# Optimization experiments

Hardware: AMD Instinct MI355X
Metric: run time of the kernel (lower is better)

The kernel has to match this reference:

```python
import math
import jax, jax.numpy as jnp
import numpy as np

WS = (8, 7, 7)   # window_size (d, h, w)
SS = (4, 3, 3)   # shift_size
NH = 4           # num_heads
DIM = 128


def _rel_position_index(ws):
    # [N*N] int index into the (2wd-1)(2wh-1)(2ww-1) bias table
    cd, ch, cw = np.arange(ws[0]), np.arange(ws[1]), np.arange(ws[2])
    coords = np.stack(np.meshgrid(cd, ch, cw, indexing='ij')).reshape(3, -1)  # [3, N]
    rel = (coords[:, :, None] - coords[:, None, :]).transpose(1, 2, 0)        # [N, N, 3]
    rel[..., 0] += ws[0] - 1
    rel[..., 1] += ws[1] - 1
    rel[..., 2] += ws[2] - 1
    rel[..., 0] *= (2 * ws[1] - 1) * (2 * ws[2] - 1)
    rel[..., 1] *= (2 * ws[2] - 1)
    return rel.sum(-1).reshape(-1)


def _rel_coords_table(ws):
    # [(2wd-1)(2wh-1)(2ww-1), 3] log-spaced continuous coords (Swin v2)
    rd = np.arange(-(ws[0] - 1), ws[0], dtype=np.float32)
    rh = np.arange(-(ws[1] - 1), ws[1], dtype=np.float32)
    rw = np.arange(-(ws[2] - 1), ws[2], dtype=np.float32)
    t = np.stack(np.meshgrid(rd, rh, rw, indexing='ij')).transpose(1, 2, 3, 0)  # [Td,Th,Tw,3]
    t[..., 0] /= ws[0] - 1
    t[..., 1] /= ws[1] - 1
    t[..., 2] /= ws[2] - 1
    t *= 8.0
    t = np.sign(t) * np.log2(np.abs(t) + 1.0) / 3.0
    return t.reshape(-1, 3)


_REL_INDEX = _rel_position_index(WS)
_COORDS = jnp.asarray(_rel_coords_table(WS))


def _attn_mask(pD, pH, pW, ws, ss):
    img = np.zeros((pD, pH, pW), np.float32)
    sl = lambda w, s: (slice(0, -w), slice(-w, -s), slice(-s, None))
    cnt = 0
    for d in sl(ws[0], ss[0]):
        for h in sl(ws[1], ss[1]):
            for w in sl(ws[2], ss[2]):
                img[d, h, w] = cnt
                cnt += 1
    m = img.reshape(pD // ws[0], ws[0], pH // ws[1], ws[1], pW // ws[2], ws[2])
    m = m.transpose(0, 2, 4, 1, 3, 5).reshape(-1, ws[0] * ws[1] * ws[2])  # [nWin, N]
    diff = m[:, None, :] - m[:, :, None]
    return jnp.asarray(np.where(diff != 0, -100.0, 0.0).astype(np.float32))


def setup_inputs() -> dict:
    key = jax.random.key(0)
    ks = jax.random.split(key, 6)
    B, D, H, W, C = 1, 16, 56, 56, DIM
    g = lambda k, shp, sc: jax.random.normal(k, shp, dtype=jnp.float32) * sc
    return {
        'x': g(ks[0], (B, D, H, W, C), 1.0),
        'qkv_weight': g(ks[1], (3 * C, C), 0.02),
        'qkv_bias': jnp.zeros((3 * C,), jnp.float32),
        'proj_weight': g(ks[2], (C, C), 0.02),
        'proj_bias': jnp.zeros((C,), jnp.float32),
        'logit_scale': jnp.full((NH, 1, 1), float(np.log(10.0)), jnp.float32),
        'cpb_w1': g(ks[3], (512, 3), 0.02),
        'cpb_b1': jnp.zeros((512,), jnp.float32),
        'cpb_w2': g(ks[4], (NH, 512), 0.02),
    }


def reference(x, qkv_weight, qkv_bias, proj_weight, proj_bias,
              logit_scale, cpb_w1, cpb_b1, cpb_w2):
    B, D, H, W, C = x.shape
    wd, wh, ww = WS
    hd = C // NH
    pad_d, pad_h, pad_w = (-D) % wd, (-H) % wh, (-W) % ww
    x = jnp.pad(x, ((0, 0), (0, pad_d), (0, pad_h), (0, pad_w), (0, 0)))
    pD, pH, pW = D + pad_d, H + pad_h, W + pad_w
    ss = [0 if WS[i] >= (pD, pH, pW)[i] else SS[i] for i in range(3)]
    shifted = sum(ss) > 0
    if shifted:
        x = jnp.roll(x, (-ss[0], -ss[1], -ss[2]), axis=(1, 2, 3))
    nd, nh, nw = pD // wd, pH // wh, pW // ww
    nWin, N = nd * nh * nw, wd * wh * ww
    # window partition -> [B*nWin, N, C]
    xw = x.reshape(B, nd, wd, nh, wh, nw, ww, C).transpose(0, 1, 3, 5, 2, 4, 6, 7)
    xw = xw.reshape(B * nWin, N, C)
    # qkv with k-bias zeroed (Swin v2 cosine attention)
    qb = qkv_bias.at[C:2 * C].set(0.0)
    qkv = (xw @ qkv_weight.T + qb).reshape(B * nWin, N, 3, NH, hd).transpose(2, 0, 3, 1, 4)
    q, k, v = qkv[0], qkv[1], qkv[2]   # each [B*nWin, NH, N, hd]
    qn = q / jnp.maximum(jnp.linalg.norm(q, axis=-1, keepdims=True), 1e-12)
    kn = k / jnp.maximum(jnp.linalg.norm(k, axis=-1, keepdims=True), 1e-12)
    attn = jnp.einsum('bhnd,bhmd->bhnm', qn, kn)
    scale = jnp.exp(jnp.minimum(logit_scale, math.log(100.0)))  # [NH,1,1]
    attn = attn * scale
    # continuous relative position bias
    table = jax.nn.relu(_COORDS @ cpb_w1.T + cpb_b1) @ cpb_w2.T  # [T, NH]
    bias = table[_REL_INDEX].reshape(N, N, NH).transpose(2, 0, 1)
    bias = 16.0 * jax.nn.sigmoid(bias)
    attn = attn + bias[None]
    if shifted:
        mask = _attn_mask(pD, pH, pW, WS, ss)  # [nWin, N, N]
        attn = attn.reshape(B, nWin, NH, N, N) + mask[None, :, None]
        attn = attn.reshape(B * nWin, NH, N, N)
    attn = jax.nn.softmax(attn, axis=-1)
    out = jnp.einsum('bhnm,bhmd->bhnd', attn, v).transpose(0, 2, 1, 3).reshape(B * nWin, N, C)
    out = out @ proj_weight.T + proj_bias
    # window reverse -> [B, pD, pH, pW, C]
    out = out.reshape(B, nd, nh, nw, wd, wh, ww, C).transpose(0, 1, 4, 2, 5, 3, 6, 7)
    out = out.reshape(B, pD, pH, pW, C)
    if shifted:
        out = jnp.roll(out, tuple(ss), axis=(1, 2, 3))
    return out[:, :D, :H, :W, :]
```

## Files before the change

kernel.cpp:

```cpp
#include <hip/hip_runtime.h>
#include <hip/hip_bf16.h>

typedef unsigned short u16;
typedef unsigned int   u32;
typedef float f32x4  __attribute__((ext_vector_type(4)));
typedef short bf16x8 __attribute__((ext_vector_type(8)));

#define DI __device__ __forceinline__

constexpr int TBL  = 2535;
constexpr int NTOK = 50176;
constexpr float L2E = 1.4426950408889634f;

constexpr int WB_QW = 0;
constexpr int WB_PW = 49152;
constexpr int WB_QB = 65536;
constexpr int WB_PB = 65920;
constexpr int WB_TOT = 66048;

DI float b2f(u16 u){ return __uint_as_float(((u32)u)<<16); }
DI u16 f2b(float f){
  u32 u = __float_as_uint(f);
  return (u16)((u + 0x7fffu + ((u>>16)&1u)) >> 16);
}
DI float ldf(const void* p, int i, int isf32){
  return isf32 ? ((const float*)p)[i] : b2f(((const u16*)p)[i]);
}
DI f32x4 mfma32(bf16x8 a, bf16x8 b, f32x4 c){
  return __builtin_amdgcn_mfma_f32_16x16x32_bf16(a, b, c, 0, 0, 0);
}
DI u32 cvtpk(float lo, float hi){
  u32 r;
  asm("v_cvt_pk_bf16_f32 %0, %1, %2" : "=v"(r) : "v"(lo), "v"(hi));
  return r;
}
DI float vexp2(float x){
  float r;
  asm("v_exp_f32 %0, %1" : "=v"(r) : "v"(x));
  return r;
}
DI int detect_f32(const void* x, int lane){
  u32 w = ((const u32*)x)[lane];
  u16 lo = (u16)w;
  u32 e = (lo >> 7) & 0xFF;
  int wild = (lo != 0 && (e >= 143 || e <= 111)) ? 1 : 0;
  unsigned long long m = __ballot(wild);
  return __popcll(m) > 16;
}

__global__ void k_cpb(const void* __restrict__ w1, const void* __restrict__ b1,
                      const void* __restrict__ w2, const void* __restrict__ x,
                      const void* __restrict__ qw, const void* __restrict__ pw,
                      const void* __restrict__ qb, const void* __restrict__ pb,
                      u16* __restrict__ wb, float* __restrict__ table16){
  const int lane = threadIdx.x;
  const int isf32 = detect_f32(x, lane);
  {
    int gid = blockIdx.x*64 + lane;
    if (gid < WB_TOT){
      const void* src; int off;
      if (gid < WB_PW)      { src = qw; off = gid; }
      else if (gid < WB_QB) { src = pw; off = gid - WB_PW; }
      else if (gid < WB_PB) { src = qb; off = gid - WB_QB; }
      else                  { src = pb; off = gid - WB_PB; }
      wb[gid] = isf32 ? f2b(((const float*)src)[off]) : ((const u16*)src)[off];
    }
  }
  int t = blockIdx.x;
  int i = t/169; int r = t - i*169; int j = r/13; int k = r - j*13;
  float v0 = 8.f*(float)(i-7)/7.f, v1 = 8.f*(float)(j-6)/6.f, v2 = 8.f*(float)(k-6)/6.f;
  float c0 = copysignf(log2f(fabsf(v0)+1.f)*(1.f/3.f), v0);
  float c1 = copysignf(log2f(fabsf(v1)+1.f)*(1.f/3.f), v1);
  float c2 = copysignf(log2f(fabsf(v2)+1.f)*(1.f/3.f), v2);
  float a0=0.f,a1=0.f,a2=0.f,a3=0.f;
  for (int hh = lane; hh < 512; hh += 64){
    float a = c0*ldf(w1,hh*3,isf32) + c1*ldf(w1,hh*3+1,isf32)
            + c2*ldf(w1,hh*3+2,isf32) + ldf(b1,hh,isf32);
    a = fmaxf(a, 0.f);
    a0 += a*ldf(w2,hh,isf32);       a1 += a*ldf(w2,512+hh,isf32);
    a2 += a*ldf(w2,1024+hh,isf32);  a3 += a*ldf(w2,1536+hh,isf32);
  }
  #pragma unroll
  for (int off=32; off; off>>=1){
    a0 += __shfl_xor(a0, off); a1 += __shfl_xor(a1, off);
    a2 += __shfl_xor(a2, off); a3 += __shfl_xor(a3, off);
  }
  if (lane==0){
    table16[t]       = (16.f/(1.f+__expf(-a0)) - 15.f)*L2E;
    table16[TBL+t]   = (16.f/(1.f+__expf(-a1)) - 15.f)*L2E;
    table16[2*TBL+t] = (16.f/(1.f+__expf(-a2)) - 15.f)*L2E;
    table16[3*TBL+t] = (16.f/(1.f+__expf(-a3)) - 15.f)*L2E;
  }
}

__global__ void k_bias(const float* __restrict__ table16, float* __restrict__ bias16){
  int n = blockIdx.x, h = blockIdx.y;
  int td = n/49; int r2 = n - td*49; int th = r2/7; int tw = r2 - th*7;
  const float* tb = table16 + h*TBL;
  float* o = bias16 + ((size_t)h*392 + n)*392;
  for (int m = threadIdx.x; m < 392; m += 128){
    int sd = m/49; int q2 = m - sd*49; int sh = q2/7; int sw = q2 - sh*7;
    int idx = (td - sd + 7)*169 + (th - sh + 6)*13 + (tw - sw + 6);
    o[m] = tb[idx];
  }
}

__global__ __launch_bounds__(256,4) void k_qkv(const void* __restrict__ x,
    const u16* __restrict__ wb, const void* __restrict__ lsc,
    u16* __restrict__ qkvbuf){
  __shared__ __align__(16) u16 Ws[128*136];
  const int tid = threadIdx.x;
  const int lane = tid & 63;
  const int isf32 = detect_f32(x, lane);
  const int wave = tid>>6;
  const int c = lane & 15, g = lane >> 4;
  const int tokbase = blockIdx.x*64 + wave*16;
  bf16x8 ka[4];
  {
    int gtok = tokbase + c;
    int win = gtok/392, tt = gtok - win*392;
    int dwi = win>>6, hwi = (win>>3)&7, wwi = win&7;
    int td = tt/49; int r2 = tt - td*49; int th = r2/7; int tw = r2 - th*7;
    int pd = dwi*8 + td + 4; if (pd >= 16) pd -= 16;
    int ph = hwi*7 + th + 3; if (ph >= 56) ph -= 56;
    int pw = wwi*7 + tw + 3; if (pw >= 56) pw -= 56;
    size_t rowb = (size_t)((pd*56 + ph)*56 + pw)*128;
    if (isf32){
      const float* xr = (const float*)x + rowb + g*8;
      #pragma unroll
      for (int kk=0; kk<4; ++kk){
        float4 f0 = *(const float4*)(xr + kk*32);
        float4 f1 = *(const float4*)(xr + kk*32 + 4);
        uint4 p;
        p.x = cvtpk(f0.x, f0.y);  p.y = cvtpk(f0.z, f0.w);
        p.z = cvtpk(f1.x, f1.y);  p.w = cvtpk(f1.z, f1.w);
        ka[kk] = *(bf16x8*)&p;
      }
    } else {
      const u16* xr = (const u16*)x + rowb + g*8;
      #pragma unroll
      for (int kk=0; kk<4; ++kk)
        ka[kk] = *(const bf16x8*)(xr + kk*32);
    }
  }
  float sl2e[4];
  #pragma unroll
  for (int h2=0; h2<4; ++h2){
    float ls = ldf(lsc, h2, isf32);
    sl2e[h2] = __expf(fminf(ls, 4.60517019f)) * L2E;
  }
  for (int which = 0; which < 3; ++which){
    if (which) __syncthreads();
    {
      int orow = tid>>1, c2 = (tid&1)*64;
      const uint4* src = (const uint4*)(wb + WB_QW + (size_t)(which*128 + orow)*128 + c2);
      #pragma unroll
      for (int u=0; u<8; ++u) *(uint4*)&Ws[orow*136 + c2 + u*8] = src[u];
    }
    __syncthreads();
    f32x4 acc[8];
    #pragma unroll
    for (int nt=0; nt<8; ++nt) acc[nt] = 0.f;
    #pragma unroll
    for (int nt=0; nt<8; ++nt){
      #pragma unroll
      for (int kk=0; kk<4; ++kk){
        bf16x8 wf = *(const bf16x8*)&Ws[(nt*16 + c)*136 + kk*32 + g*8];
        acc[nt] = mfma32(ka[kk], wf, acc[nt]);
      }
    }
    if (which != 1){
      #pragma unroll
      for (int nt=0; nt<8; ++nt){
        float bv = b2f(wb[WB_QB + which*128 + nt*16 + c]);
        #pragma unroll
        for (int r=0;r<4;++r) acc[nt][r] += bv;
      }
    }
    if (which < 2){
      #pragma unroll
      for (int h2=0; h2<4; ++h2){
        f32x4 ss;
        #pragma unroll
        for (int r=0;r<4;++r)
          ss[r] = acc[2*h2][r]*acc[2*h2][r] + acc[2*h2+1][r]*acc[2*h2+1][r];
        #pragma unroll
        for (int off=1; off<16; off<<=1){
          #pragma unroll
          for (int r=0;r<4;++r) ss[r] += __shfl_xor(ss[r], off);
        }
        #pragma unroll
        for (int r=0;r<4;++r){
          float rn = rsqrtf(fmaxf(ss[r], 1e-24f));
          if (which == 0) rn *= sl2e[h2];
          acc[2*h2][r]   *= rn;
          acc[2*h2+1][r] *= rn;
        }
      }
    }
    #pragma unroll
    for (int nt=0; nt<8; ++nt){
      int oc = nt*16 + c;
      int head = oc >> 5, chb = oc & 31;
      #pragma unroll
      for (int r=0;r<4;++r){
        int t = tokbase + 4*g + r;
        qkvbuf[((size_t)(which*4+head)*NTOK + t)*32 + chb] = f2b(acc[nt][r]);
      }
    }
  }
}

DI bf16x8 ldK(const u16* klds, int jt, int c, int g){
  return *(const bf16x8*)&klds[(jt*16 + c)*40 + g*8];
}
DI float4 ldB(const float* brow, int jt, int g){
  int mbc = jt*16 + 4*g; if (mbc > 388) mbc = 388;
  return *(const float4*)(brow + mbc);
}
DI int4 ldC(const int* cnt, int jt, int g){
  int mbc = jt*16 + 4*g; if (mbc > 388) mbc = 388;
  return *(const int4*)&cnt[mbc];
}

#define QKT_BODY(JJ, TAIL, KF, BA, BB, CM, JT) do { \
  f32x4 tz = {0.f,0.f,0.f,0.f}; \
  f32x4 ta = mfma32(KF, qfa, tz); \
  f32x4 tb = mfma32(KF, qfb, tz); \
  float pa0 = vexp2(ta[0] + BA.x), pa1 = vexp2(ta[1] + BA.y); \
  float pa2 = vexp2(ta[2] + BA.z), pa3 = vexp2(ta[3] + BA.w); \
  float pb0 = vexp2(tb[0] + BB.x), pb1 = vexp2(tb[1] + BB.y); \
  float pb2 = vexp2(tb[2] + BB.z), pb3 = vexp2(tb[3] + BB.w); \
  if (MIXED){ \
    if (CM.x != cnA) pa0 = 0.f;  if (CM.y != cnA) pa1 = 0.f; \
    if (CM.z != cnA) pa2 = 0.f;  if (CM.w != cnA) pa3 = 0.f; \
    if (CM.x != cnB) pb0 = 0.f;  if (CM.y != cnB) pb1 = 0.f; \
    if (CM.z != cnB) pb2 = 0.f;  if (CM.w != cnB) pb3 = 0.f; \
  } \
  if (TAIL){ \
    const int mb = (JT)*16 + 4*g; \
    if (mb > 388){ pa0=0.f; pa1=0.f; pa2=0.f; pa3=0.f; \
                   pb0=0.f; pb1=0.f; pb2=0.f; pb3=0.f; } \
  } \
  uint2 wva, wvb; \
  wva.x = cvtpk(pa0,pa1); wva.y = cvtpk(pa2,pa3); \
  wvb.x = cvtpk(pb0,pb1); wvb.y = cvtpk(pb2,pb3); \
  *(uint2*)&psA[c*20 + (JJ)*8 + 2*g] = wva; \
  *(uint2*)&psB[c*20 + (JJ)*8 + 2*g] = wvb; \
} while(0)

#define PV_PAIR(MC) do { \
  bf16x8 pfa = *(const bf16x8*)&psA[c*20 + 4*g]; \
  bf16x8 pfb = *(const bf16x8*)&psB[c*20 + 4*g]; \
  bf16x8 va = *(const bf16x8*)&vT[c*424 + (MC)*32 + g*8]; \
  bf16x8 vb = *(const bf16x8*)&vT[(16+c)*424 + (MC)*32 + g*8]; \
  o0a = mfma32(va, pfa, o0a); o1a = mfma32(vb, pfa, o1a); o2a = mfma32(ones, pfa, o2a); \
  o0b = mfma32(va, pfb, o0b); o1b = mfma32(vb, pfb, o1b); o2b = mfma32(ones, pfb, o2b); \
} while(0)

template<bool MIXED>
DI void attn_main(const u16* __restrict__ qg, const float* __restrict__ bias_h,
                  const u16* klds, const u16* vT, u32* psA, u32* psB, const int* cnt,
                  u16* __restrict__ aout, int win, int h, int wave, int lane){
  const int c = lane & 15, g = lane >> 4;
  const short ob = 0x3F80;
  const bf16x8 ones = {ob,ob,ob,ob,ob,ob,ob,ob};
  const int4 zc = {0,0,0,0};
  for (int pp = wave; pp < 13; pp += 8){
    const int rta = 2*pp;
    const int rtb = (pp < 12) ? (2*pp+1) : 24;
    const bool hasB = (pp < 12);
    const int nbA = rta*16, nbB = rtb*16;
    const int ncA = (nbA + c < 392) ? (nbA + c) : 391;
    const int ncB = (nbB + c < 392) ? (nbB + c) : 391;
    const bf16x8 qfa = *(const bf16x8*)(qg + (size_t)ncA*32 + g*8);
    const bf16x8 qfb = *(const bf16x8*)(qg + (size_t)ncB*32 + g*8);
    const int cnA = MIXED ? cnt[ncA] : 0;
    const int cnB = MIXED ? cnt[ncB] : 0;
    const float* browA = bias_h + (size_t)ncA*392;
    const float* browB = bias_h + (size_t)ncB*392;
    f32x4 o0a = {0.f,0.f,0.f,0.f}, o1a = o0a, o2a = o0a;
    f32x4 o0b = o0a, o1b = o0a, o2b = o0a;
    bf16x8 kf0 = ldK(klds, 0, c, g);
    float4 ba0 = ldB(browA, 0, g), bb0 = ldB(browB, 0, g);
    int4   cm0 = MIXED ? ldC(cnt, 0, g) : zc;
    for (int mc = 0; mc < 12; ++mc){
      const int jt1 = 2*mc + 1, jt2 = 2*mc + 2;
      bf16x8 kf1 = ldK(klds, jt1, c, g);
      float4 ba1 = ldB(browA, jt1, g), bb1 = ldB(browB, jt1, g);
      int4   cm1 = MIXED ? ldC(cnt, jt1, g) : zc;
      QKT_BODY(0, false, kf0, ba0, bb0, cm0, 2*mc);
      kf0 = ldK(klds, jt2, c, g);
      ba0 = ldB(browA, jt2, g); bb0 = ldB(browB, jt2, g);
      cm0 = MIXED ? ldC(cnt, jt2, g) : zc;
      QKT_BODY(1, false, kf1, ba1, bb1, cm1, jt1);
      PV_PAIR(mc);
    }
    QKT_BODY(0, true, kf0, ba0, bb0, cm0, 24);
    { uint2 zz; zz.x = 0u; zz.y = 0u;
      *(uint2*)&psA[c*20 + 8 + 2*g] = zz;
      *(uint2*)&psB[c*20 + 8 + 2*g] = zz; }
    PV_PAIR(12);
    const float rva = 1.f / o2a[0];
    const float rvb = 1.f / o2b[0];
    uint2 wa, wb2;
    wa.x  = cvtpk(o0a[0]*rva, o0a[1]*rva);  wa.y  = cvtpk(o0a[2]*rva, o0a[3]*rva);
    wb2.x = cvtpk(o1a[0]*rva, o1a[1]*rva);  wb2.y = cvtpk(o1a[2]*rva, o1a[3]*rva);
    *(uint2*)&psA[c*20 + 2*g]     = wa;
    *(uint2*)&psA[c*20 + 8 + 2*g] = wb2;
    wa.x  = cvtpk(o0b[0]*rvb, o0b[1]*rvb);  wa.y  = cvtpk(o0b[2]*rvb, o0b[3]*rvb);
    wb2.x = cvtpk(o1b[0]*rvb, o1b[1]*rvb);  wb2.y = cvtpk(o1b[2]*rvb, o1b[3]*rvb);
    *(uint2*)&psB[c*20 + 2*g]     = wa;
    *(uint2*)&psB[c*20 + 8 + 2*g] = wb2;
    const int orow = lane>>2, oq = lane&3;
    uint4 ova = *(const uint4*)&psA[orow*20 + 4*oq];
    const int nA = nbA + orow;
    if (nA < 392)
      *(uint4*)(aout + ((size_t)(win*392 + nA))*128 + h*32 + oq*8) = ova;
    if (hasB){
      uint4 ovb = *(const uint4*)&psB[orow*20 + 4*oq];
      const int nB = nbB + orow;
      if (nB < 392)
        *(uint4*)(aout + ((size_t)(win*392 + nB))*128 + h*32 + oq*8) = ovb;
    }
  }
}

__global__ __launch_bounds__(512,4) void k_attn(const u16* __restrict__ qkv,
    const float* __restrict__ bias16, u16* __restrict__ aout){
  __shared__ __align__(16) u16 klds[400*40];
  __shared__ __align__(16) u16 vT[32*424];
  __shared__ __align__(16) u32 ps[8][640];
  __shared__ __align__(16) int cnt[400];
  const int tid = threadIdx.x;
  const int win = blockIdx.x, h = blockIdx.y;
  const int dwi = win>>6, hwi = (win>>3)&7, wwi = win&7;
  const u16* qg = qkv + ((size_t)(0*4 + h)*NTOK + (size_t)win*392)*32;
  const u16* kg = qkv + ((size_t)(1*4 + h)*NTOK + (size_t)win*392)*32;
  const u16* vg = qkv + ((size_t)(2*4 + h)*NTOK + (size_t)win*392)*32;
  for (int idx = tid; idx < 1600; idx += 512){
    const int row = idx>>2, q = idx&3;
    uint4 a = {0,0,0,0};
    if (row < 392) a = *(const uint4*)(kg + (size_t)row*32 + q*8);
    *(uint4*)&klds[row*40 + q*8] = a;
  }
  for (int idx = tid; idx < 784; idx += 512){
    const int mg = idx>>3, cg = idx&7;
    uint2 v0 = *(const uint2*)(vg + (size_t)(4*mg+0)*32 + cg*4);
    uint2 v1 = *(const uint2*)(vg + (size_t)(4*mg+1)*32 + cg*4);
    uint2 v2 = *(const uint2*)(vg + (size_t)(4*mg+2)*32 + cg*4);
    uint2 v3 = *(const uint2*)(vg + (size_t)(4*mg+3)*32 + cg*4);
    u16 e0[4], e1[4], e2[4], e3[4];
    e0[0]=(u16)v0.x; e0[1]=(u16)(v0.x>>16); e0[2]=(u16)v0.y; e0[3]=(u16)(v0.y>>16);
    e1[0]=(u16)v1.x; e1[1]=(u16)(v1.x>>16); e1[2]=(u16)v1.y; e1[3]=(u16)(v1.y>>16);
    e2[0]=(u16)v2.x; e2[1]=(u16)(v2.x>>16); e2[2]=(u16)v2.y; e2[3]=(u16)(v2.y>>16);
    e3[0]=(u16)v3.x; e3[1]=(u16)(v3.x>>16); e3[2]=(u16)v3.y; e3[3]=(u16)(v3.y>>16);
    #pragma unroll
    for (int cc=0; cc<4; ++cc){
      ushort4 w = make_ushort4(e0[cc], e1[cc], e2[cc], e3[cc]);
      *(ushort4*)&vT[(cg*4+cc)*424 + 4*mg] = w;
    }
  }
  for (int idx = tid; idx < 1024; idx += 512){
    int ch = idx>>5, mm = 392 + (idx&31);
    vT[ch*424 + mm] = 0;
  }
  for (int t2 = tid; t2 < 400; t2 += 512){
    int row = (t2 < 392) ? t2 : 391;
    int td = row/49; int r2 = row - td*49; int th = r2/7; int tw = r2 - th*7;
    int gd = dwi*8 + td, gh = hwi*7 + th, gw = wwi*7 + tw;
    int rd = (gd < 8) ? 0 : ((gd < 12) ? 1 : 2);
    int rh = (gh < 49) ? 0 : ((gh < 53) ? 1 : 2);
    int rw = (gw < 49) ? 0 : ((gw < 53) ? 1 : 2);
    cnt[t2] = rd*9 + rh*3 + rw;
  }
  __syncthreads();
  const int wave = tid>>6, lane = tid&63;
  u32* psA = &ps[wave][0];
  u32* psB = &ps[wave][320];
  const float* bias_h = bias16 + (size_t)h*153664;
  const bool uniform = (dwi == 0) && (hwi < 7) && (wwi < 7);
  if (uniform)
    attn_main<false>(qg, bias_h, klds, vT, psA, psB, cnt, aout, win, h, wave, lane);
  else
    attn_main<true >(qg, bias_h, klds, vT, psA, psB, cnt, aout, win, h, wave, lane);
}

__global__ __launch_bounds__(256,2) void k_proj(const u16* __restrict__ ain,
    const u16* __restrict__ wb, const void* __restrict__ x, void* __restrict__ out){
  __shared__ __align__(16) u16 As[64*136];
  __shared__ __align__(16) u16 Ws[128*136];
  const int tid = threadIdx.x;
  const int lane = tid & 63;
  const int isf32 = detect_f32(x, lane);
  const int tokbase0 = blockIdx.x*64;
  {
    int trow = tid>>2, cq = (tid&3)*32;
    const uint4* src = (const uint4*)(ain + (size_t)(tokbase0+trow)*128 + cq);
    #pragma unroll
    for (int u=0; u<4; ++u) *(uint4*)&As[trow*136 + cq + u*8] = src[u];
  }
  {
    int orow = tid>>1, c2 = (tid&1)*64;
    const uint4* src = (const uint4*)(wb + WB_PW + (size_t)orow*128 + c2);
    #pragma unroll
    for (int u=0; u<8; ++u) *(uint4*)&Ws[orow*136 + c2 + u*8] = src[u];
  }
  __syncthreads();
  const int wave = tid>>6;
  const int c = lane & 15, g = lane >> 4;
  bf16x8 ka[4];
  #pragma unroll
  for (int kk=0; kk<4; ++kk)
    ka[kk] = *(const bf16x8*)&As[(wave*16 + c)*136 + kk*32 + g*8];
  f32x4 acc[8];
  #pragma unroll
  for (int nt=0; nt<8; ++nt) acc[nt] = 0.f;
  #pragma unroll
  for (int nt=0; nt<8; ++nt){
    #pragma unroll
    for (int kk=0; kk<4; ++kk){
      bf16x8 wf = *(const bf16x8*)&Ws[(nt*16 + c)*136 + kk*32 + g*8];
      acc[nt] = mfma32(ka[kk], wf, acc[nt]);
    }
  }
  if (isf32){
    __syncthreads();
    float* WsF = (float*)Ws;
    #pragma unroll
    for (int nt=0; nt<8; ++nt){
      float bv = b2f(wb[WB_PB + nt*16 + c]);
      #pragma unroll
      for (int r=0;r<4;++r)
        WsF[(wave*16 + 4*g + r)*128 + nt*16 + c] = acc[nt][r] + bv;
    }
    __syncthreads();
    const int tok = tid>>2, q4 = tid&3;
    int gtok = tokbase0 + tok;
    int win = gtok/392, tt = gtok - win*392;
    int dwi = win>>6, hwi = (win>>3)&7, wwi = win&7;
    int td = tt/49; int r2 = tt - td*49; int th = r2/7; int tw = r2 - th*7;
    int pd = dwi*8 + td + 4; if (pd >= 16) pd -= 16;
    int ph = hwi*7 + th + 3; if (ph >= 56) ph -= 56;
    int pwx = wwi*7 + tw + 3; if (pwx >= 56) pwx -= 56;
    size_t po = (size_t)((pd*56 + ph)*56 + pwx)*128;
    const float4* srcv = (const float4*)&WsF[tok*128 + q4*32];
    float4* dst = (float4*)((float*)out + po + q4*32);
    #pragma unroll
    for (int i=0;i<8;++i) dst[i] = srcv[i];
  } else {
    const int tokbase = tokbase0 + wave*16;
    size_t po[4];
    #pragma unroll
    for (int r=0;r<4;++r){
      int gtok = tokbase + 4*g + r;
      int win = gtok/392, tt = gtok - win*392;
      int dwi = win>>6, hwi = (win>>3)&7, wwi = win&7;
      int td = tt/49; int r2 = tt - td*49; int th = r2/7; int tw = r2 - th*7;
      int pd = dwi*8 + td + 4; if (pd >= 16) pd -= 16;
      int ph = hwi*7 + th + 3; if (ph >= 56) ph -= 56;
      int pwx = wwi*7 + tw + 3; if (pwx >= 56) pwx -= 56;
      po[r] = (size_t)((pd*56 + ph)*56 + pwx)*128;
    }
    #pragma unroll
    for (int nt=0; nt<8; ++nt){
      int oc = nt*16 + c;
      float bv = b2f(wb[WB_PB + oc]);
      #pragma unroll
      for (int r=0;r<4;++r)
        ((u16*)out)[po[r] + oc] = f2b(acc[nt][r] + bv);
    }
  }
}

extern "C" void kernel_launch(void* const* d_in, const int* in_sizes, int n_in,
                              void* d_out, int out_size, void* d_ws, size_t ws_size,
                              hipStream_t stream){
  const void* x      = d_in[0];
  const void* qkv_w  = d_in[1];
  const void* qkv_b  = d_in[2];
  const void* proj_w = d_in[3];
  const void* proj_b = d_in[4];
  const void* lsc    = d_in[5];
  const void* cpb_w1 = d_in[6];
  const void* cpb_b1 = d_in[7];
  const void* cpb_w2 = d_in[8];
  char* ws = (char*)d_ws;
  float* table16 = (float*)(ws);
  float* bias16  = (float*)(ws + 40960);
  u16*   wb      = (u16*)(ws + 2499584);
  u16*   qkvbuf  = (u16*)(ws + 2631680);
  u16*   attnout = (u16*)(ws + 41166848);

  k_cpb <<<TBL, 64, 0, stream>>>(cpb_w1, cpb_b1, cpb_w2, x,
                                 qkv_w, proj_w, qkv_b, proj_b, wb, table16);
  k_bias<<<dim3(392,4), 128, 0, stream>>>(table16, bias16);
  k_qkv <<<784, 256, 0, stream>>>(x, wb, lsc, qkvbuf);
  k_attn<<<dim3(128,4), 512, 0, stream>>>(qkvbuf, bias16, attnout);
  k_proj<<<784, 256, 0, stream>>>(attnout, wb, x, d_out);
}
```

Measured before the change: 94.89 us.

## Drop materialized bias matrix; gather bias from table via packed per-token indices

Removes the k_bias kernel and its per-head 392x392 float bias buffer. The attention kernel now packs each token's table offset and mask region id into one shared int, and gathers bias values straight from the small relative-position table using index differences. This cuts a kernel launch and the global-memory traffic of writing and reading the full bias matrix, at the cost of four scalar gathers per float4. k_proj also now loads its A fragments directly from global into registers, skipping the LDS staging, and raises its occupancy hint from 2 to 4.

```diff
diff --git a/kernel.cpp b/kernel.cpp
--- a/kernel.cpp
+++ b/kernel.cpp
@@ -90,18 +90,6 @@
     table16[TBL+t]   = (16.f/(1.f+__expf(-a1)) - 15.f)*L2E;
     table16[2*TBL+t] = (16.f/(1.f+__expf(-a2)) - 15.f)*L2E;
     table16[3*TBL+t] = (16.f/(1.f+__expf(-a3)) - 15.f)*L2E;
-  }
-}
-
-__global__ void k_bias(const float* __restrict__ table16, float* __restrict__ bias16){
-  int n = blockIdx.x, h = blockIdx.y;
-  int td = n/49; int r2 = n - td*49; int th = r2/7; int tw = r2 - th*7;
-  const float* tb = table16 + h*TBL;
-  float* o = bias16 + ((size_t)h*392 + n)*392;
-  for (int m = threadIdx.x; m < 392; m += 128){
-    int sd = m/49; int q2 = m - sd*49; int sh = q2/7; int sw = q2 - sh*7;
-    int idx = (td - sd + 7)*169 + (th - sh + 6)*13 + (tw - sw + 6);
-    o[m] = tb[idx];
   }
 }
 
@@ -214,13 +202,17 @@
 DI bf16x8 ldK(const u16* klds, int jt, int c, int g){
   return *(const bf16x8*)&klds[(jt*16 + c)*40 + g*8];
 }
-DI float4 ldB(const float* brow, int jt, int g){
+DI int4 ldP(const int* pk, int jt, int g){
   int mbc = jt*16 + 4*g; if (mbc > 388) mbc = 388;
-  return *(const float4*)(brow + mbc);
-}
-DI int4 ldC(const int* cnt, int jt, int g){
-  int mbc = jt*16 + 4*g; if (mbc > 388) mbc = 388;
-  return *(const int4*)&cnt[mbc];
+  return *(const int4*)&pk[mbc];
+}
+DI float4 gatherB(const float* tn, int4 pm){
+  float4 b;
+  b.x = tn[-(pm.x & 0xffff)];
+  b.y = tn[-(pm.y & 0xffff)];
+  b.z = tn[-(pm.z & 0xffff)];
+  b.w = tn[-(pm.w & 0xffff)];
+  return b;
 }
 
 #define QKT_BODY(JJ, TAIL, KF, BA, BB, CM, JT) do { \
@@ -232,10 +224,10 @@
   float pb0 = vexp2(tb[0] + BB.x), pb1 = vexp2(tb[1] + BB.y); \
   float pb2 = vexp2(tb[2] + BB.z), pb3 = vexp2(tb[3] + BB.w); \
   if (MIXED){ \
-    if (CM.x != cnA) pa0 = 0.f;  if (CM.y != cnA) pa1 = 0.f; \
-    if (CM.z != cnA) pa2 = 0.f;  if (CM.w != cnA) pa3 = 0.f; \
-    if (CM.x != cnB) pb0 = 0.f;  if (CM.y != cnB) pb1 = 0.f; \
-    if (CM.z != cnB) pb2 = 0.f;  if (CM.w != cnB) pb3 = 0.f; \
+    if ((CM.x>>16) != cnA) pa0 = 0.f;  if ((CM.y>>16) != cnA) pa1 = 0.f; \
+    if ((CM.z>>16) != cnA) pa2 = 0.f;  if ((CM.w>>16) != cnA) pa3 = 0.f; \
+    if ((CM.x>>16) != cnB) pb0 = 0.f;  if ((CM.y>>16) != cnB) pb1 = 0.f; \
+    if ((CM.z>>16) != cnB) pb2 = 0.f;  if ((CM.w>>16) != cnB) pb3 = 0.f; \
   } \
   if (TAIL){ \
     const int mb = (JT)*16 + 4*g; \
@@ -259,13 +251,12 @@
 } while(0)
 
 template<bool MIXED>
-DI void attn_main(const u16* __restrict__ qg, const float* __restrict__ bias_h,
-                  const u16* klds, const u16* vT, u32* psA, u32* psB, const int* cnt,
+DI void attn_main(const u16* __restrict__ qg, const float* __restrict__ tbh,
+                  const u16* klds, const u16* vT, u32* psA, u32* psB, const int* pk,
                   u16* __restrict__ aout, int win, int h, int wave, int lane){
   const int c = lane & 15, g = lane >> 4;
   const short ob = 0x3F80;
   const bf16x8 ones = {ob,ob,ob,ob,ob,ob,ob,ob};
-  const int4 zc = {0,0,0,0};
   for (int pp = wave; pp < 13; pp += 8){
     const int rta = 2*pp;
     const int rtb = (pp < 12) ? (2*pp+1) : 24;
@@ -275,28 +266,28 @@
     const int ncB = (nbB + c < 392) ? (nbB + c) : 391;
     const bf16x8 qfa = *(const bf16x8*)(qg + (size_t)ncA*32 + g*8);
     const bf16x8 qfb = *(const bf16x8*)(qg + (size_t)ncB*32 + g*8);
-    const int cnA = MIXED ? cnt[ncA] : 0;
-    const int cnB = MIXED ? cnt[ncB] : 0;
-    const float* browA = bias_h + (size_t)ncA*392;
-    const float* browB = bias_h + (size_t)ncB*392;
+    const int pkA = pk[ncA], pkB = pk[ncB];
+    const int cnA = pkA >> 16, cnB = pkB >> 16;
+    const float* tnA = tbh + (pkA & 0xffff);
+    const float* tnB = tbh + (pkB & 0xffff);
     f32x4 o0a = {0.f,0.f,0.f,0.f}, o1a = o0a, o2a = o0a;
     f32x4 o0b = o0a, o1b = o0a, o2b = o0a;
     bf16x8 kf0 = ldK(klds, 0, c, g);
-    float4 ba0 = ldB(browA, 0, g), bb0 = ldB(browB, 0, g);
-    int4   cm0 = MIXED ? ldC(cnt, 0, g) : zc;
+    int4   pm0 = ldP(pk, 0, g);
+    float4 ba0 = gatherB(tnA, pm0), bb0 = gatherB(tnB, pm0);
     for (int mc = 0; mc < 12; ++mc){
       const int jt1 = 2*mc + 1, jt2 = 2*mc + 2;
       bf16x8 kf1 = ldK(klds, jt1, c, g);
-      float4 ba1 = ldB(browA, jt1, g), bb1 = ldB(browB, jt1, g);
-      int4   cm1 = MIXED ? ldC(cnt, jt1, g) : zc;
-      QKT_BODY(0, false, kf0, ba0, bb0, cm0, 2*mc);
+      int4   pm1 = ldP(pk, jt1, g);
+      float4 ba1 = gatherB(tnA, pm1), bb1 = gatherB(tnB, pm1);
+      QKT_BODY(0, false, kf0, ba0, bb0, pm0, 2*mc);
       kf0 = ldK(klds, jt2, c, g);
-      ba0 = ldB(browA, jt2, g); bb0 = ldB(browB, jt2, g);
-      cm0 = MIXED ? ldC(cnt, jt2, g) : zc;
-      QKT_BODY(1, false, kf1, ba1, bb1, cm1, jt1);
+      pm0 = ldP(pk, jt2, g);
+      ba0 = gatherB(tnA, pm0); bb0 = gatherB(tnB, pm0);
+      QKT_BODY(1, false, kf1, ba1, bb1, pm1, jt1);
       PV_PAIR(mc);
     }
-    QKT_BODY(0, true, kf0, ba0, bb0, cm0, 24);
+    QKT_BODY(0, true, kf0, ba0, bb0, pm0, 24);
     { uint2 zz; zz.x = 0u; zz.y = 0u;
       *(uint2*)&psA[c*20 + 8 + 2*g] = zz;
       *(uint2*)&psB[c*20 + 8 + 2*g] = zz; }
@@ -327,11 +318,11 @@
 }
 
 __global__ __launch_bounds__(512,4) void k_attn(const u16* __restrict__ qkv,
-    const float* __restrict__ bias16, u16* __restrict__ aout){
+    const float* __restrict__ table16, u16* __restrict__ aout){
   __shared__ __align__(16) u16 klds[400*40];
   __shared__ __align__(16) u16 vT[32*424];
   __shared__ __align__(16) u32 ps[8][640];
-  __shared__ __align__(16) int cnt[400];
+  __shared__ __align__(16) int pk[400];
   const int tid = threadIdx.x;
   const int win = blockIdx.x, h = blockIdx.y;
   const int dwi = win>>6, hwi = (win>>3)&7, wwi = win&7;
@@ -372,33 +363,38 @@
     int rd = (gd < 8) ? 0 : ((gd < 12) ? 1 : 2);
     int rh = (gh < 49) ? 0 : ((gh < 53) ? 1 : 2);
     int rw = (gw < 49) ? 0 : ((gw < 53) ? 1 : 2);
-    cnt[t2] = rd*9 + rh*3 + rw;
+    int cntv = rd*9 + rh*3 + rw;
+    int mpart = td*169 + th*13 + tw;
+    pk[t2] = mpart | (cntv << 16);
   }
   __syncthreads();
   const int wave = tid>>6, lane = tid&63;
   u32* psA = &ps[wave][0];
   u32* psB = &ps[wave][320];
-  const float* bias_h = bias16 + (size_t)h*153664;
+  const float* tbh = table16 + h*TBL + 1267;
   const bool uniform = (dwi == 0) && (hwi < 7) && (wwi < 7);
   if (uniform)
-    attn_main<false>(qg, bias_h, klds, vT, psA, psB, cnt, aout, win, h, wave, lane);
+    attn_main<false>(qg, tbh, klds, vT, psA, psB, pk, aout, win, h, wave, lane);
   else
-    attn_main<true >(qg, bias_h, klds, vT, psA, psB, cnt, aout, win, h, wave, lane);
-}
-
-__global__ __launch_bounds__(256,2) void k_proj(const u16* __restrict__ ain,
+    attn_main<true >(qg, tbh, klds, vT, psA, psB, pk, aout, win, h, wave, lane);
+}
+
+__global__ __launch_bounds__(256,4) void k_proj(const u16* __restrict__ ain,
     const u16* __restrict__ wb, const void* __restrict__ x, void* __restrict__ out){
-  __shared__ __align__(16) u16 As[64*136];
   __shared__ __align__(16) u16 Ws[128*136];
   const int tid = threadIdx.x;
   const int lane = tid & 63;
   const int isf32 = detect_f32(x, lane);
+  const int wave = tid>>6;
+  const int c = lane & 15, g = lane >> 4;
   const int tokbase0 = blockIdx.x*64;
+  const int tokbase = tokbase0 + wave*16;
+  bf16x8 ka[4];
   {
-    int trow = tid>>2, cq = (tid&3)*32;
-    const uint4* src = (const uint4*)(ain + (size_t)(tokbase0+trow)*128 + cq);
-    #pragma unroll
-    for (int u=0; u<4; ++u) *(uint4*)&As[trow*136 + cq + u*8] = src[u];
+    const u16* ar = ain + (size_t)(tokbase + c)*128 + g*8;
+    #pragma unroll
+    for (int kk=0; kk<4; ++kk)
+      ka[kk] = *(const bf16x8*)(ar + kk*32);
   }
   {
     int orow = tid>>1, c2 = (tid&1)*64;
@@ -407,12 +403,6 @@
     for (int u=0; u<8; ++u) *(uint4*)&Ws[orow*136 + c2 + u*8] = src[u];
   }
   __syncthreads();
-  const int wave = tid>>6;
-  const int c = lane & 15, g = lane >> 4;
-  bf16x8 ka[4];
-  #pragma unroll
-  for (int kk=0; kk<4; ++kk)
-    ka[kk] = *(const bf16x8*)&As[(wave*16 + c)*136 + kk*32 + g*8];
   f32x4 acc[8];
   #pragma unroll
   for (int nt=0; nt<8; ++nt) acc[nt] = 0.f;
@@ -449,7 +439,6 @@
     #pragma unroll
     for (int i=0;i<8;++i) dst[i] = srcv[i];
   } else {
-    const int tokbase = tokbase0 + wave*16;
     size_t po[4];
     #pragma unroll
     for (int r=0;r<4;++r){
@@ -487,15 +476,13 @@
   const void* cpb_w2 = d_in[8];
   char* ws = (char*)d_ws;
   float* table16 = (float*)(ws);
-  float* bias16  = (float*)(ws + 40960);
-  u16*   wb      = (u16*)(ws + 2499584);
-  u16*   qkvbuf  = (u16*)(ws + 2631680);
-  u16*   attnout = (u16*)(ws + 41166848);
+  u16*   wb      = (u16*)(ws + 40960);
+  u16*   qkvbuf  = (u16*)(ws + 173056);
+  u16*   attnout = (u16*)(ws + 38708224);
 
   k_cpb <<<TBL, 64, 0, stream>>>(cpb_w1, cpb_b1, cpb_w2, x,
                                  qkv_w, proj_w, qkv_b, proj_b, wb, table16);
-  k_bias<<<dim3(392,4), 128, 0, stream>>>(table16, bias16);
   k_qkv <<<784, 256, 0, stream>>>(x, wb, lsc, qkvbuf);
-  k_attn<<<dim3(128,4), 512, 0, stream>>>(qkvbuf, bias16, attnout);
+  k_attn<<<dim3(128,4), 512, 0, stream>>>(qkvbuf, table16, attnout);
   k_proj<<<784, 256, 0, stream>>>(attnout, wb, x, d_out);
 }
```

Result: slower. 106.5 us (+12.2%).
